# Kernel tuning notes

Measured on AMD Instinct MI355X. Metric: run time of the kernel, lower is better.

Reference implementation:

```python
import jax, jax.numpy as jnp
import numpy as np

S, B = 16384, 1
E = 2048          # encoder_hidden_size * num_enc_direction
H = 1024          # decoder_hidden_size
L = 2             # num_layer_dec
C = 5             # num_classes


def setup_inputs() -> dict:
    key = jax.random.key(0)
    ks = jax.random.split(key, 16)
    s = lambda fan_in: 1.0 / np.sqrt(fan_in)
    inp = {
        "encoder_hiddens": jax.random.normal(ks[0], (S, B, E), jnp.float32),
        "hidden": jax.random.normal(ks[1], (L, B, H), jnp.float32),
        "c": jax.random.normal(ks[2], (L, B, H), jnp.float32),
        # attn_alpha: Linear(2H + E, 1)
        "attn_w": jax.random.uniform(ks[3], (1, 2 * H + E), jnp.float32, -s(2 * H + E), s(2 * H + E)),
        "attn_b": jax.random.uniform(ks[4], (1,), jnp.float32, -s(2 * H + E), s(2 * H + E)),
        # LSTM layer 0: input E -> H
        "w_ih_l0": jax.random.uniform(ks[5], (4 * H, E), jnp.float32, -s(H), s(H)),
        "w_hh_l0": jax.random.uniform(ks[6], (4 * H, H), jnp.float32, -s(H), s(H)),
        "b_ih_l0": jax.random.uniform(ks[7], (4 * H,), jnp.float32, -s(H), s(H)),
        "b_hh_l0": jax.random.uniform(ks[8], (4 * H,), jnp.float32, -s(H), s(H)),
        # LSTM layer 1: input H -> H
        "w_ih_l1": jax.random.uniform(ks[9], (4 * H, H), jnp.float32, -s(H), s(H)),
        "w_hh_l1": jax.random.uniform(ks[10], (4 * H, H), jnp.float32, -s(H), s(H)),
        "b_ih_l1": jax.random.uniform(ks[11], (4 * H,), jnp.float32, -s(H), s(H)),
        "b_hh_l1": jax.random.uniform(ks[12], (4 * H,), jnp.float32, -s(H), s(H)),
        # fc: Linear(H, C)
        "fc_w": jax.random.uniform(ks[13], (C, H), jnp.float32, -s(H), s(H)),
        "fc_b": jax.random.uniform(ks[14], (C,), jnp.float32, -s(H), s(H)),
    }
    return inp


def _lstm_cell(x, h, c, w_ih, w_hh, b_ih, b_hh):
    # PyTorch gate order: i, f, g, o
    gates = x @ w_ih.T + b_ih + h @ w_hh.T + b_hh  # [B, 4H]
    i, f, g, o = jnp.split(gates, 4, axis=-1)
    c2 = jax.nn.sigmoid(f) * c + jax.nn.sigmoid(i) * jnp.tanh(g)
    h2 = jax.nn.sigmoid(o) * jnp.tanh(c2)
    return h2, c2


def reference(encoder_hiddens, hidden, c, attn_w, attn_b,
              w_ih_l0, w_hh_l0, b_ih_l0, b_hh_l0,
              w_ih_l1, w_hh_l1, b_ih_l1, b_hh_l1,
              fc_w, fc_b):
    h0, c0 = hidden[0], c[0]  # [B, H]
    # Vectorized per-timestep attn_alpha(concat(h0, c0, enc_i)):
    # split attn_w columns over [h0 | c0 | enc] and fuse the static part.
    w_h, w_c, w_e = attn_w[:, :H], attn_w[:, H:2 * H], attn_w[:, 2 * H:]
    static = h0 @ w_h.T + c0 @ w_c.T + attn_b            # [B, 1]
    scores = jnp.einsum('sbe,oe->sbo', encoder_hiddens, w_e) + static  # [S, B, 1]
    # Original applies softmax over dim=1 of a [B=1, 1] tensor per step -> all ones.
    attn = jax.nn.softmax(scores, axis=-1)               # [S, B, 1], identically 1.0
    # bmm(enc[B,E,S], attn[B,S,1]) == weighted sum over S
    attn_applied = jnp.einsum('sbe,sb->be', encoder_hiddens, attn[..., 0])  # [B, E]

    # 2-layer LSTM, single timestep
    h1, c1 = _lstm_cell(attn_applied, hidden[0], c[0], w_ih_l0, w_hh_l0, b_ih_l0, b_hh_l0)
    h2, c2 = _lstm_cell(h1, hidden[1], c[1], w_ih_l1, w_hh_l1, b_ih_l1, b_hh_l1)

    out = h2  # [B, H] == out.view(1*B, H)
    return out @ fc_w.T + fc_b  # [B, C]
```

## Files before the change

kernel.cpp:

```cpp
#include <hip/hip_runtime.h>
#include <hip/hip_bf16.h>
#include <math.h>

#define S_LEN 16384
#define E_DIM 2048
#define H_DIM 1024
#define G_DIM 4096
#define C_DIM 5

#define CS_CHUNKS 512
#define CS_ROWS   (S_LEN / CS_CHUNKS)

#define WS_PART   0
#define WS_COLSUM (WS_PART + CS_CHUNKS * E_DIM)
#define WS_G0     (WS_COLSUM + E_DIM)
#define WS_G1     (WS_G0 + G_DIM)

__device__ __forceinline__ float wave_sum(float v) {
#pragma unroll
  for (int off = 32; off > 0; off >>= 1) v += __shfl_down(v, off);
  return v;
}

__device__ __forceinline__ float dot4(float4 a, float4 b) {
  return a.x * b.x + a.y * b.y + a.z * b.z + a.w * b.w;
}

__device__ __forceinline__ float sigm(float x) { return 1.f / (1.f + expf(-x)); }

__global__ __launch_bounds__(256) void colsum_partial_k(
    const float4* __restrict__ enc, float4* __restrict__ part) {
  const int E4 = E_DIM / 4;
  int colgroup = blockIdx.x & 1;
  int chunk = blockIdx.x >> 1;
  int e4 = colgroup * 256 + threadIdx.x;
  float4 acc = {0.f, 0.f, 0.f, 0.f};
  size_t base = (size_t)chunk * CS_ROWS * E4 + e4;
#pragma unroll 8
  for (int r = 0; r < CS_ROWS; ++r) {
    float4 v = enc[base + (size_t)r * E4];
    acc.x += v.x; acc.y += v.y; acc.z += v.z; acc.w += v.w;
  }
  part[(size_t)chunk * E4 + e4] = acc;
}

__global__ __launch_bounds__(256) void colsum_final_k(
    const float* __restrict__ part, float* __restrict__ colsum) {
  __shared__ float red[4][64];
  int lane = threadIdx.x & 63;
  int grp = threadIdx.x >> 6;
  int col = blockIdx.x * 64 + lane;
  float acc = 0.f;
  int c0 = grp * (CS_CHUNKS / 4);
#pragma unroll 8
  for (int ch = c0; ch < c0 + CS_CHUNKS / 4; ++ch)
    acc += part[(size_t)ch * E_DIM + col];
  red[grp][lane] = acc;
  __syncthreads();
  if (threadIdx.x < 64) {
    float s = (red[0][lane] + red[1][lane]) + (red[2][lane] + red[3][lane]);
    colsum[col] = s;
  }
}

__global__ __launch_bounds__(256) void gates0_k(
    const float4* __restrict__ w_ih, const float4* __restrict__ w_hh,
    const float* __restrict__ b_ih, const float* __restrict__ b_hh,
    const float4* __restrict__ x, const float4* __restrict__ h,
    float* __restrict__ gates) {
  int wave = threadIdx.x >> 6;
  int lane = threadIdx.x & 63;
  int row = blockIdx.x * 4 + wave;

  float acc = 0.f;
  const float4* wi = w_ih + (size_t)row * 512;
#pragma unroll
  for (int k = lane; k < 512; k += 64) acc += dot4(wi[k], x[k]);
  const float4* wh = w_hh + (size_t)row * 256;
#pragma unroll
  for (int k = lane; k < 256; k += 64) acc += dot4(wh[k], h[k]);
  acc = wave_sum(acc);
  if (lane == 0) gates[row] = acc + b_ih[row] + b_hh[row];
}

__global__ __launch_bounds__(256) void gates1_cell0_k(
    const float* __restrict__ g0, const float* __restrict__ c0,
    const float4* __restrict__ w_ih, const float4* __restrict__ w_hh,
    const float* __restrict__ b_ih, const float* __restrict__ b_hh,
    const float4* __restrict__ h,
    float* __restrict__ gates) {
  __shared__ __align__(16) float h1s[H_DIM];
#pragma unroll
  for (int k = 0; k < 4; ++k) {
    int j = threadIdx.x + 256 * k;
    float ig = g0[j], fg = g0[H_DIM + j], gg = g0[2 * H_DIM + j],
          og = g0[3 * H_DIM + j];
    float c2 = sigm(fg) * c0[j] + sigm(ig) * tanhf(gg);
    h1s[j] = sigm(og) * tanhf(c2);
  }
  __syncthreads();

  int wave = threadIdx.x >> 6;
  int lane = threadIdx.x & 63;
  int row = blockIdx.x * 4 + wave;
  const float4* h1s4 = (const float4*)h1s;

  float acc = 0.f;
  const float4* wi = w_ih + (size_t)row * 256;
#pragma unroll
  for (int k = lane; k < 256; k += 64) acc += dot4(wi[k], h1s4[k]);
  const float4* wh = w_hh + (size_t)row * 256;
#pragma unroll
  for (int k = lane; k < 256; k += 64) acc += dot4(wh[k], h[k]);
  acc = wave_sum(acc);
  if (lane == 0) gates[row] = acc + b_ih[row] + b_hh[row];
}

__global__ __launch_bounds__(512) void fc_cell1_k(
    const float* __restrict__ g1, const float* __restrict__ c1,
    const float4* __restrict__ fc_w, const float* __restrict__ fc_b,
    float* __restrict__ out) {
  __shared__ __align__(16) float h2s[H_DIM];
#pragma unroll
  for (int k = 0; k < 2; ++k) {
    int j = threadIdx.x + 512 * k;
    float ig = g1[j], fg = g1[H_DIM + j], gg = g1[2 * H_DIM + j],
          og = g1[3 * H_DIM + j];
    float c2 = sigm(fg) * c1[j] + sigm(ig) * tanhf(gg);
    h2s[j] = sigm(og) * tanhf(c2);
  }
  __syncthreads();

  int wave = threadIdx.x >> 6;
  int lane = threadIdx.x & 63;
  if (wave < C_DIM) {
    const float4* h24 = (const float4*)h2s;
    const float4* wr = fc_w + (size_t)wave * 256;
    float acc = 0.f;
#pragma unroll
    for (int k = lane; k < 256; k += 64) acc += dot4(wr[k], h24[k]);
    acc = wave_sum(acc);
    if (lane == 0) out[wave] = acc + fc_b[wave];
  }
}

extern "C" void kernel_launch(void* const* d_in, const int* in_sizes, int n_in,
                              void* d_out, int out_size, void* d_ws, size_t ws_size,
                              hipStream_t stream) {
  const float* enc     = (const float*)d_in[0];
  const float* hidden  = (const float*)d_in[1];
  const float* c_in    = (const float*)d_in[2];
  const float* w_ih_l0 = (const float*)d_in[5];
  const float* w_hh_l0 = (const float*)d_in[6];
  const float* b_ih_l0 = (const float*)d_in[7];
  const float* b_hh_l0 = (const float*)d_in[8];
  const float* w_ih_l1 = (const float*)d_in[9];
  const float* w_hh_l1 = (const float*)d_in[10];
  const float* b_ih_l1 = (const float*)d_in[11];
  const float* b_hh_l1 = (const float*)d_in[12];
  const float* fc_w    = (const float*)d_in[13];
  const float* fc_b    = (const float*)d_in[14];

  float* ws = (float*)d_ws;
  float* part   = ws + WS_PART;
  float* colsum = ws + WS_COLSUM;
  float* g0     = ws + WS_G0;
  float* g1     = ws + WS_G1;
  float* out    = (float*)d_out;

  colsum_partial_k<<<2 * CS_CHUNKS, 256, 0, stream>>>(
      (const float4*)enc, (float4*)part);
  colsum_final_k<<<E_DIM / 64, 256, 0, stream>>>(part, colsum);

  gates0_k<<<G_DIM / 4, 256, 0, stream>>>(
      (const float4*)w_ih_l0, (const float4*)w_hh_l0, b_ih_l0, b_hh_l0,
      (const float4*)colsum, (const float4*)hidden, g0);

  gates1_cell0_k<<<G_DIM / 4, 256, 0, stream>>>(
      g0, c_in,
      (const float4*)w_ih_l1, (const float4*)w_hh_l1, b_ih_l1, b_hh_l1,
      (const float4*)(hidden + H_DIM), g1);

  fc_cell1_k<<<1, 512, 0, stream>>>(
      g1, c_in + H_DIM, (const float4*)fc_w, fc_b, out);
}
```

Baseline: 55.40 us.

## Fuse hidden-state GEMVs into the encoder colsum streaming kernel

New measurement: 56.70 us. +2.4%, slower.

```diff
diff --git a/kernel.cpp b/kernel.cpp
--- a/kernel.cpp
+++ b/kernel.cpp
@@ -13,35 +13,60 @@
 
 #define WS_PART   0
 #define WS_COLSUM (WS_PART + CS_CHUNKS * E_DIM)
-#define WS_G0     (WS_COLSUM + E_DIM)
+#define WS_HH0    (WS_COLSUM + E_DIM)
+#define WS_HH1    (WS_HH0 + G_DIM)
+#define WS_G0     (WS_HH1 + G_DIM)
 #define WS_G1     (WS_G0 + G_DIM)
+
+typedef float fvec4 __attribute__((ext_vector_type(4)));
 
 __device__ __forceinline__ float wave_sum(float v) {
 #pragma unroll
   for (int off = 32; off > 0; off >>= 1) v += __shfl_down(v, off);
   return v;
 }
-
 __device__ __forceinline__ float dot4(float4 a, float4 b) {
   return a.x * b.x + a.y * b.y + a.z * b.z + a.w * b.w;
 }
-
 __device__ __forceinline__ float sigm(float x) { return 1.f / (1.f + expf(-x)); }
 
-__global__ __launch_bounds__(256) void colsum_partial_k(
-    const float4* __restrict__ enc, float4* __restrict__ part) {
-  const int E4 = E_DIM / 4;
-  int colgroup = blockIdx.x & 1;
-  int chunk = blockIdx.x >> 1;
-  int e4 = colgroup * 256 + threadIdx.x;
-  float4 acc = {0.f, 0.f, 0.f, 0.f};
-  size_t base = (size_t)chunk * CS_ROWS * E4 + e4;
+__global__ __launch_bounds__(256) void stream_k(
+    const fvec4* __restrict__ enc, const float4* __restrict__ hidden,
+    const float4* __restrict__ w_hh_l0,
+    const float* __restrict__ b_ih_l0, const float* __restrict__ b_hh_l0,
+    const float4* __restrict__ w_hh_l1,
+    const float* __restrict__ b_ih_l1, const float* __restrict__ b_hh_l1,
+    fvec4* __restrict__ part, float* __restrict__ hh0,
+    float* __restrict__ hh1) {
+  int b = blockIdx.x;
+  if (b < 1024) {
+    int e4 = (b & 1) * 256 + threadIdx.x;
+    int chunk = b >> 1;
+    fvec4 acc = {0.f, 0.f, 0.f, 0.f};
+    size_t base = (size_t)chunk * CS_ROWS * 512 + e4;
 #pragma unroll 8
-  for (int r = 0; r < CS_ROWS; ++r) {
-    float4 v = enc[base + (size_t)r * E4];
-    acc.x += v.x; acc.y += v.y; acc.z += v.z; acc.w += v.w;
-  }
-  part[(size_t)chunk * E4 + e4] = acc;
+    for (int r = 0; r < CS_ROWS; ++r) {
+      fvec4 v = __builtin_nontemporal_load(&enc[base + (size_t)r * 512]);
+      acc += v;
+    }
+    part[(size_t)chunk * 512 + e4] = acc;
+  } else {
+    int which = (b >= 2048) ? 1 : 0;
+    int wave = threadIdx.x >> 6;
+    int lane = threadIdx.x & 63;
+    int row = ((b & 1023) << 2) + wave;
+    const float4* w = (which ? w_hh_l1 : w_hh_l0) + (size_t)row * 256;
+    const float4* h = hidden + (which ? 256 : 0);
+    float a = 0.f;
+#pragma unroll
+    for (int k = lane; k < 256; k += 64) a += dot4(w[k], h[k]);
+    a = wave_sum(a);
+    if (lane == 0) {
+      float bias = which ? (b_ih_l1[row] + b_hh_l1[row])
+                         : (b_ih_l0[row] + b_hh_l0[row]);
+      (which ? hh1 : hh0)[row] = a + bias;
+    }
+  }
 }
 
 __global__ __launch_bounds__(256) void colsum_final_k(
@@ -64,31 +89,23 @@
 }
 
 __global__ __launch_bounds__(256) void gates0_k(
-    const float4* __restrict__ w_ih, const float4* __restrict__ w_hh,
-    const float* __restrict__ b_ih, const float* __restrict__ b_hh,
-    const float4* __restrict__ x, const float4* __restrict__ h,
-    float* __restrict__ gates) {
+    const float4* __restrict__ w_ih, const float4* __restrict__ x,
+    const float* __restrict__ hh0, float* __restrict__ g0) {
   int wave = threadIdx.x >> 6;
   int lane = threadIdx.x & 63;
   int row = blockIdx.x * 4 + wave;
-
-  float acc = 0.f;
   const float4* wi = w_ih + (size_t)row * 512;
-#pragma unroll
-  for (int k = lane; k < 512; k += 64) acc += dot4(wi[k], x[k]);
-  const float4* wh = w_hh + (size_t)row * 256;
-#pragma unroll
-  for (int k = lane; k < 256; k += 64) acc += dot4(wh[k], h[k]);
-  acc = wave_sum(acc);
-  if (lane == 0) gates[row] = acc + b_ih[row] + b_hh[row];
+  float a = 0.f;
+#pragma unroll
+  for (int k = lane; k < 512; k += 64) a += dot4(wi[k], x[k]);
+  a = wave_sum(a);
+  if (lane == 0) g0[row] = a + hh0[row];
 }
 
 __global__ __launch_bounds__(256) void gates1_cell0_k(
     const float* __restrict__ g0, const float* __restrict__ c0,
-    const float4* __restrict__ w_ih, const float4* __restrict__ w_hh,
-    const float* __restrict__ b_ih, const float* __restrict__ b_hh,
-    const float4* __restrict__ h,
-    float* __restrict__ gates) {
+    const float4* __restrict__ w_ih, const float* __restrict__ hh1,
+    float* __restrict__ g1) {
   __shared__ __align__(16) float h1s[H_DIM];
 #pragma unroll
   for (int k = 0; k < 4; ++k) {
@@ -103,17 +120,13 @@
   int wave = threadIdx.x >> 6;
   int lane = threadIdx.x & 63;
   int row = blockIdx.x * 4 + wave;
-  const float4* h1s4 = (const float4*)h1s;
-
-  float acc = 0.f;
+  const float4* h14 = (const float4*)h1s;
   const float4* wi = w_ih + (size_t)row * 256;
-#pragma unroll
-  for (int k = lane; k < 256; k += 64) acc += dot4(wi[k], h1s4[k]);
-  const float4* wh = w_hh + (size_t)row * 256;
-#pragma unroll
-  for (int k = lane; k < 256; k += 64) acc += dot4(wh[k], h[k]);
-  acc = wave_sum(acc);
-  if (lane == 0) gates[row] = acc + b_ih[row] + b_hh[row];
+  float a = 0.f;
+#pragma unroll
+  for (int k = lane; k < 256; k += 64) a += dot4(wi[k], h14[k]);
+  a = wave_sum(a);
+  if (lane == 0) g1[row] = a + hh1[row];
 }
 
 __global__ __launch_bounds__(512) void fc_cell1_k(
@@ -164,22 +177,25 @@
   float* ws = (float*)d_ws;
   float* part   = ws + WS_PART;
   float* colsum = ws + WS_COLSUM;
+  float* hh0    = ws + WS_HH0;
+  float* hh1    = ws + WS_HH1;
   float* g0     = ws + WS_G0;
   float* g1     = ws + WS_G1;
   float* out    = (float*)d_out;
 
-  colsum_partial_k<<<2 * CS_CHUNKS, 256, 0, stream>>>(
-      (const float4*)enc, (float4*)part);
+  stream_k<<<3072, 256, 0, stream>>>(
+      (const fvec4*)enc, (const float4*)hidden,
+      (const float4*)w_hh_l0, b_ih_l0, b_hh_l0,
+      (const float4*)w_hh_l1, b_ih_l1, b_hh_l1,
+      (fvec4*)part, hh0, hh1);
+
   colsum_final_k<<<E_DIM / 64, 256, 0, stream>>>(part, colsum);
 
   gates0_k<<<G_DIM / 4, 256, 0, stream>>>(
-      (const float4*)w_ih_l0, (const float4*)w_hh_l0, b_ih_l0, b_hh_l0,
-      (const float4*)colsum, (const float4*)hidden, g0);
+      (const float4*)w_ih_l0, (const float4*)colsum, hh0, g0);
 
   gates1_cell0_k<<<G_DIM / 4, 256, 0, stream>>>(
-      g0, c_in,
-      (const float4*)w_ih_l1, (const float4*)w_hh_l1, b_ih_l1, b_hh_l1,
-      (const float4*)(hidden + H_DIM), g1);
+      g0, c_in, (const float4*)w_ih_l1, hh1, g1);
 
   fc_cell1_k<<<1, 512, 0, stream>>>(
       g1, c_in + H_DIM, (const float4*)fc_w, fc_b, out);
```
